# Kernel optimization log

Measured on AMD Instinct MI355X. Metric: run time of the kernel, lower is better.

The kernel has to match this reference:

```python
import jax, jax.numpy as jnp
import numpy as np

B = 512       # number of graphs
MAX_N = 128   # pad length (>= max(num_atoms))
D = 256       # emb_dim


def setup_inputs() -> dict:
    key = jax.random.key(0)
    ks = jax.random.split(key, 20)
    num_atoms_np = np.full(B, 80, dtype=np.int64)
    num_atoms_np[: B // 2] = 112
    num_atoms_np[B // 2 :] = 48
    total = int(num_atoms_np.sum())  # 40960, static
    scale = 1.0 / np.sqrt(D)

    def lin_w(k):
        return jax.random.normal(k, (D, D), jnp.float32) * scale

    inp = {
        'rep_2d': jax.random.normal(ks[0], (total, D), jnp.float32),
        'rep_3d': jax.random.normal(ks[1], (total, D), jnp.float32),
        'num_atoms': jnp.asarray(num_atoms_np),
        # mha_2d_3d (queries from 2d, keys/values from 3d)
        'wq23': lin_w(ks[2]), 'bq23': jnp.zeros((D,), jnp.float32),
        'wk23': lin_w(ks[3]), 'bk23': jnp.zeros((D,), jnp.float32),
        'wv23': lin_w(ks[4]), 'bv23': jnp.zeros((D,), jnp.float32),
        # mha_3d_2d (queries from 3d, keys/values from 2d)
        'wq32': lin_w(ks[5]), 'bq32': jnp.zeros((D,), jnp.float32),
        'wk32': lin_w(ks[6]), 'bk32': jnp.zeros((D,), jnp.float32),
        'wv32': lin_w(ks[7]), 'bv32': jnp.zeros((D,), jnp.float32),
        # per-branch Linear (normalizer=Identity) + GELU
        'wm23': lin_w(ks[8]), 'bm23': jnp.zeros((D,), jnp.float32),
        'wm32': lin_w(ks[9]), 'bm32': jnp.zeros((D,), jnp.float32),
    }
    return inp


def _variadic_to_padded(flat, num_atoms):
    # flat: [total, D] -> padded [B, MAX_N, D], mask [B, MAX_N] (True = valid)
    cum = jnp.cumsum(num_atoms)
    offsets = cum - num_atoms
    pos = jnp.arange(MAX_N)
    mask = pos[None, :] < num_atoms[:, None]
    idx = jnp.where(mask, offsets[:, None] + pos[None, :], 0)
    padded = flat[idx] * mask[..., None].astype(flat.dtype)
    return padded, mask


def _padded_to_variadic(padded, num_atoms, total):
    # padded: [B, MAX_N, D] -> flat [total, D]
    cum = jnp.cumsum(num_atoms)
    t = jnp.arange(total)
    b = jnp.searchsorted(cum, t, side='right')
    i = t - (cum - num_atoms)[b]
    return padded[b, i]


def _cross_attn(q_in, kv_in, mask, wq, bq, wk, bk, wv, bv):
    # single-head scaled dot-product cross-attention, key-side padding mask
    q = q_in @ wq.T + bq
    k = kv_in @ wk.T + bk
    v = kv_in @ wv.T + bv
    s = jnp.einsum('bqd,bkd->bqk', q, k) / jnp.sqrt(jnp.asarray(D, q.dtype))
    s = jnp.where(mask[:, None, :], s, jnp.asarray(-1e9, s.dtype))
    a = jax.nn.softmax(s, axis=-1)
    return jnp.einsum('bqk,bkd->bqd', a, v)


def reference(rep_2d, rep_3d, num_atoms,
              wq23, bq23, wk23, bk23, wv23, bv23,
              wq32, bq32, wk32, bk32, wv32, bv32,
              wm23, bm23, wm32, bm32):
    total = rep_2d.shape[0]
    p2d, mask = _variadic_to_padded(rep_2d, num_atoms)
    p3d, _ = _variadic_to_padded(rep_3d, num_atoms)
    x2d = _cross_attn(p2d, p3d, mask, wq23, bq23, wk23, bk23, wv23, bv23)
    x3d = _cross_attn(p3d, p2d, mask, wq32, bq32, wk32, bk32, wv32, bv32)
    x2d = _padded_to_variadic(x2d, num_atoms, total)
    x3d = _padded_to_variadic(x3d, num_atoms, total)
    out2d = jax.nn.gelu(x2d @ wm23.T + bm23, approximate=False)
    out3d = jax.nn.gelu(x3d @ wm32.T + bm32, approximate=False)
    return (out2d, out3d)
```

## Files before the change

kernel.cpp:

```cpp
#include <hip/hip_runtime.h>
#include <hip/hip_bf16.h>
#include <cstdint>


typedef short s16x8 __attribute__((ext_vector_type(8)));
typedef float f32x4 __attribute__((ext_vector_type(4)));

__device__ __forceinline__ s16x8 cvt8(const float* p) {
  float4 a0 = *(const float4*)p, a1 = *(const float4*)(p + 4);
  union { s16x8 v; __bf16 e[8]; } u;
  u.e[0] = (__bf16)a0.x; u.e[1] = (__bf16)a0.y; u.e[2] = (__bf16)a0.z; u.e[3] = (__bf16)a0.w;
  u.e[4] = (__bf16)a1.x; u.e[5] = (__bf16)a1.y; u.e[6] = (__bf16)a1.z; u.e[7] = (__bf16)a1.w;
  return u.v;
}
__device__ __forceinline__ float fast_gelu(float x) {
  float ax = fabsf(x);
  float t = 1.0f / (1.0f + 0.3275911f * (ax * 0.70710678f));
  float y = t * (0.254829592f + t * (-0.284496736f + t * (1.421413741f +
            t * (-1.453152027f + t * 1.061405429f))));
  float er = 1.0f - y * __expf(-0.5f * ax * ax);
  er = (x < 0.f) ? -er : er;
  return 0.5f * x * (1.0f + er);
}

__global__ void sentinel_kernel(float* out, float v) {
  if (threadIdx.x == 0 && blockIdx.x == 0) out[0] = v;
}

__global__ __launch_bounds__(512) void scan_kernel(
    const int* __restrict__ na, int* __restrict__ offs,
    int B, int total, float* out)
{
  __shared__ int s32[512];
  __shared__ int s64[512];
  const int t = threadIdx.x;
  int v32 = 0, v64 = 0;
  if (t < B) {
    v32 = na[t];
    v64 = (int)((const long long*)na)[t];
  }
  s32[t] = v32; s64[t] = v64;
  __syncthreads();
  for (int o = 1; o < 512; o <<= 1) {
    int a = (t >= o) ? s32[t - o] : 0;
    int b = (t >= o) ? s64[t - o] : 0;
    __syncthreads();
    s32[t] += a; s64[t] += b;
    __syncthreads();
  }
  int tot32 = s32[B - 1], tot64 = s64[B - 1];
  bool ok32 = (tot32 == total), ok64 = (tot64 == total);
  if (t < B) offs[t] = ok32 ? (s32[t] - v32) : ok64 ? (s64[t] - v64) : 0;
  if (t == 0) {
    offs[B] = ok32 ? tot32 : ok64 ? tot64 : 0;
    if (!ok32 && !ok64) out[0] = 31337.0f;
  }
}

__global__ __launch_bounds__(256) void cvt_kernel(
    const float* __restrict__ in, __bf16* __restrict__ out) {
  int i = (blockIdx.x * 256 + threadIdx.x) * 4;
  float4 f = *(const float4*)(in + i);
  out[i + 0] = (__bf16)f.x; out[i + 1] = (__bf16)f.y;
  out[i + 2] = (__bf16)f.z; out[i + 3] = (__bf16)f.w;
}

__global__ __launch_bounds__(256) void gemm_kernel(
    const float* __restrict__ A, const float* __restrict__ Bw,
    const float* __restrict__ bias, __bf16* __restrict__ C, int N)
{
  __shared__ __bf16 At[128 * 32];
  __shared__ __bf16 Bt[128 * 32];
  const int t = threadIdx.x;
  const int lane = t & 63, w = t >> 6;
  const int wr = w >> 1, wc = w & 1;
  const int l15 = lane & 15, l4 = lane >> 4;
  const int by = blockIdx.x, bx = blockIdx.y;

  f32x4 acc[4][4];
  for (int m = 0; m < 4; ++m)
    for (int nn = 0; nn < 4; ++nn) acc[m][nn] = (f32x4){0.f, 0.f, 0.f, 0.f};

  for (int kk = 0; kk < 256; kk += 32) {
    for (int j = 0; j < 2; ++j) {
      int c = t + j * 256;
      int row = c >> 2, off0 = (c & 3) * 8;
      *(s16x8*)(&At[row * 32 + off0]) = cvt8(A + (size_t)(by * 128 + row) * 256 + kk + off0);
      *(s16x8*)(&Bt[row * 32 + off0]) = cvt8(Bw + (size_t)(bx * 128 + row) * 256 + kk + off0);
    }
    __syncthreads();
    s16x8 af[4], bfr[4];
    for (int m = 0; m < 4; ++m)
      af[m] = *(const s16x8*)(&At[(wr * 64 + m * 16 + l15) * 32 + l4 * 8]);
    for (int nn = 0; nn < 4; ++nn)
      bfr[nn] = *(const s16x8*)(&Bt[(wc * 64 + nn * 16 + l15) * 32 + l4 * 8]);
    for (int m = 0; m < 4; ++m)
      for (int nn = 0; nn < 4; ++nn)
        acc[m][nn] = __builtin_amdgcn_mfma_f32_16x16x32_bf16(af[m], bfr[nn], acc[m][nn], 0, 0, 0);
    __syncthreads();
  }

  for (int m = 0; m < 4; ++m) {
    int row0 = by * 128 + wr * 64 + m * 16 + l4 * 4;
    for (int nn = 0; nn < 4; ++nn) {
      int col = bx * 128 + wc * 64 + nn * 16 + l15;
      float bc = bias[col];
      for (int r = 0; r < 4; ++r) {
        int row = row0 + r;
        C[(size_t)row * N + col] = (__bf16)(acc[m][nn][r] + bc);
      }
    }
  }
}

#define CTP 136
__global__ __launch_bounds__(256) void vgemm_kernel(
    const float* __restrict__ A, const float* __restrict__ Bw,
    const float* __restrict__ bias, __bf16* __restrict__ Vt, int total)
{
  __shared__ __bf16 At[128 * 32];
  __shared__ __bf16 Bt[128 * 32];
  __shared__ __bf16 Ct[128 * CTP];
  const int t = threadIdx.x;
  const int lane = t & 63, w = t >> 6;
  const int wr = w >> 1, wc = w & 1;
  const int l15 = lane & 15, l4 = lane >> 4;
  const int by = blockIdx.x, bx = blockIdx.y;

  f32x4 acc[4][4];
  for (int m = 0; m < 4; ++m)
    for (int nn = 0; nn < 4; ++nn) acc[m][nn] = (f32x4){0.f, 0.f, 0.f, 0.f};

  for (int kk = 0; kk < 256; kk += 32) {
    for (int j = 0; j < 2; ++j) {
      int c = t + j * 256;
      int row = c >> 2, off0 = (c & 3) * 8;
      *(s16x8*)(&At[row * 32 + off0]) = cvt8(A + (size_t)(by * 128 + row) * 256 + kk + off0);
      *(s16x8*)(&Bt[row * 32 + off0]) = cvt8(Bw + (size_t)(bx * 128 + row) * 256 + kk + off0);
    }
    __syncthreads();
    s16x8 af[4], bfr[4];
    for (int m = 0; m < 4; ++m)
      af[m] = *(const s16x8*)(&At[(wr * 64 + m * 16 + l15) * 32 + l4 * 8]);
    for (int nn = 0; nn < 4; ++nn)
      bfr[nn] = *(const s16x8*)(&Bt[(wc * 64 + nn * 16 + l15) * 32 + l4 * 8]);
    for (int m = 0; m < 4; ++m)
      for (int nn = 0; nn < 4; ++nn)
        acc[m][nn] = __builtin_amdgcn_mfma_f32_16x16x32_bf16(af[m], bfr[nn], acc[m][nn], 0, 0, 0);
    __syncthreads();
  }

  for (int m = 0; m < 4; ++m) {
    int rl0 = wr * 64 + m * 16 + l4 * 4;
    for (int nn = 0; nn < 4; ++nn) {
      int cl = wc * 64 + nn * 16 + l15;
      for (int r = 0; r < 4; ++r) {
        int rl = rl0 + r;
        Ct[rl * CTP + cl] = (__bf16)(acc[m][nn][r] + bias[by * 128 + rl]);
      }
    }
  }
  __syncthreads();

  for (int i = 0; i < 8; ++i) {
    int c = t + i * 256;
    int row = c >> 4, seg = c & 15;
    *(uint4*)(Vt + (size_t)(by * 128 + row) * total + bx * 128 + seg * 8) =
        *(const uint4*)(&Ct[row * CTP + seg * 8]);
  }
}

struct Attn2Args {
  const __bf16* Q[2]; const __bf16* K[2]; const __bf16* V[2];
  unsigned long long X[2];
};
#define KSTR 264
#define PSTR 136
__global__ __launch_bounds__(512, 2) void attn2_kernel(
    Attn2Args args, const int* __restrict__ offs, int total)
{
  __shared__ __bf16 smem[128 * KSTR];
  __bf16 (*Klds)[KSTR] = (__bf16(*)[KSTR])smem;
  __bf16 (*Plds)[PSTR] = (__bf16(*)[PSTR])smem;

  const int br = blockIdx.y;
  const __bf16* Q  = args.Q[br];
  const __bf16* Km = args.K[br];
  const __bf16* Vt = args.V[br];
  __bf16* X = (__bf16*)args.X[br];

  const int g = blockIdx.x;
  const int off = offs[g];
  const int n = offs[g + 1] - off;
  const int t = threadIdx.x, lane = t & 63, w = t >> 6;
  const int l15 = lane & 15, l4 = lane >> 4;
  const bool qact = (w * 16) < n;

  uint4 kst[8];
  #pragma unroll
  for (int j = 0; j < 8; ++j) {
    if (j * 16 < n) {
      int row = j * 16 + (t >> 5);
      kst[j] = *(const uint4*)((const char*)(Km + (size_t)(off + row) * 256) + (t & 31) * 16);
    }
  }
  s16x8 qf[8];
  if (qact) {
    int qr = w * 16 + l15; if (qr >= n) qr = n - 1;
    const __bf16* qp = Q + (size_t)(off + qr) * 256 + l4 * 8;
    #pragma unroll
    for (int kk = 0; kk < 8; ++kk) qf[kk] = *(const s16x8*)(qp + kk * 32);
  }
  #pragma unroll
  for (int j = 0; j < 8; ++j) {
    if (j * 16 < n) {
      int row = j * 16 + (t >> 5);
      *(uint4*)((char*)&Klds[row][0] + (t & 31) * 16) = kst[j];
    }
  }
  __syncthreads();

  f32x4 sacc[8];
  #pragma unroll
  for (int i = 0; i < 8; ++i) sacc[i] = (f32x4){0.f, 0.f, 0.f, 0.f};
  if (qact) {
    #pragma unroll
    for (int kt = 0; kt < 8; ++kt) {
      if (kt * 16 < n) {
        const __bf16* kp = &Klds[kt * 16 + l15][l4 * 8];
        #pragma unroll
        for (int kk = 0; kk < 8; ++kk) {
          s16x8 kf = *(const s16x8*)(kp + kk * 32);
          sacc[kt] = __builtin_amdgcn_mfma_f32_16x16x32_bf16(qf[kk], kf, sacc[kt], 0, 0, 0);
        }
      }
    }
  }
  __syncthreads();

  if (qact) {
    #pragma unroll
    for (int r = 0; r < 4; ++r) {
      float sv[8];
      float m = -1e30f;
      #pragma unroll
      for (int kt = 0; kt < 8; ++kt) {
        int key = kt * 16 + l15;
        float v = (key < n) ? sacc[kt][r] * 0.0625f : -1e30f;
        sv[kt] = v; m = fmaxf(m, v);
      }
      for (int o = 1; o < 16; o <<= 1) m = fmaxf(m, __shfl_xor(m, o));
      float p[8], sum = 0.f;
      #pragma unroll
      for (int kt = 0; kt < 8; ++kt) { p[kt] = __expf(sv[kt] - m); sum += p[kt]; }
      for (int o = 1; o < 16; o <<= 1) sum += __shfl_xor(sum, o);
      float inv = 1.f / sum;
      int q = w * 16 + l4 * 4 + r;
      #pragma unroll
      for (int kt = 0; kt < 8; ++kt)
        Plds[q][kt * 16 + l15] = (__bf16)(p[kt] * inv);
    }
  }
  __syncthreads();

  const int dbase = w * 32;
  f32x4 xacc[2][8];
  #pragma unroll
  for (int dt = 0; dt < 2; ++dt)
    #pragma unroll
    for (int qm = 0; qm < 8; ++qm) xacc[dt][qm] = (f32x4){0.f, 0.f, 0.f, 0.f};

  #pragma unroll
  for (int dt = 0; dt < 2; ++dt) {
    int d = dbase + dt * 16 + l15;
    s16x8 vf[4];
    #pragma unroll
    for (int ks = 0; ks < 4; ++ks) {
      if (ks * 32 < n) {
        int kc = off + ks * 32 + l4 * 8;
        if (kc > total - 8) kc = total - 8;
        vf[ks] = *(const s16x8*)(Vt + (size_t)d * total + kc);
      }
    }
    #pragma unroll
    for (int qm = 0; qm < 8; ++qm) {
      if (qm * 16 < n) {
        #pragma unroll
        for (int ks = 0; ks < 4; ++ks) {
          if (ks * 32 < n) {
            s16x8 pa = *(const s16x8*)(&Plds[qm * 16 + l15][ks * 32 + l4 * 8]);
            xacc[dt][qm] = __builtin_amdgcn_mfma_f32_16x16x32_bf16(pa, vf[ks], xacc[dt][qm], 0, 0, 0);
          }
        }
      }
    }
  }

  #pragma unroll
  for (int dt = 0; dt < 2; ++dt)
    #pragma unroll
    for (int qm = 0; qm < 8; ++qm)
      #pragma unroll
      for (int r = 0; r < 4; ++r) {
        int q = qm * 16 + l4 * 4 + r;
        if (q < n)
          X[(size_t)(off + q) * 256 + dbase + dt * 16 + l15] = (__bf16)xacc[dt][qm][r];
      }
}

struct Out2Args {
  const __bf16* A[2]; const __bf16* W[2]; const float* bias[2];
  unsigned long long C[2];
};
__global__ __launch_bounds__(256) void gemm_out2(Out2Args args)
{
  __shared__ __bf16 At[64 * 32];
  __shared__ __bf16 Bt[128 * 32];
  const int z = blockIdx.z;
  const __bf16* A  = args.A[z];
  const __bf16* W  = args.W[z];
  const float* bias = args.bias[z];
  float* C = (float*)args.C[z];

  const int t = threadIdx.x;
  const int lane = t & 63, w = t >> 6;
  const int wr = w >> 1, wc = w & 1;
  const int l15 = lane & 15, l4 = lane >> 4;
  const int by = blockIdx.x, bx = blockIdx.y;

  f32x4 acc[2][4];
  for (int m = 0; m < 2; ++m)
    for (int nn = 0; nn < 4; ++nn) acc[m][nn] = (f32x4){0.f, 0.f, 0.f, 0.f};

  for (int kk = 0; kk < 256; kk += 32) {
    {
      int row = t >> 2, off0 = (t & 3) * 8;
      *(s16x8*)(&At[row * 32 + off0]) =
          *(const s16x8*)(A + (size_t)(by * 64 + row) * 256 + kk + off0);
    }
    for (int j = 0; j < 2; ++j) {
      int c = t + j * 256;
      int row = c >> 2, off0 = (c & 3) * 8;
      *(s16x8*)(&Bt[row * 32 + off0]) =
          *(const s16x8*)(W + (size_t)(bx * 128 + row) * 256 + kk + off0);
    }
    __syncthreads();
    s16x8 af[2], bfr[4];
    for (int m = 0; m < 2; ++m)
      af[m] = *(const s16x8*)(&At[(wr * 32 + m * 16 + l15) * 32 + l4 * 8]);
    for (int nn = 0; nn < 4; ++nn)
      bfr[nn] = *(const s16x8*)(&Bt[(wc * 64 + nn * 16 + l15) * 32 + l4 * 8]);
    for (int m = 0; m < 2; ++m)
      for (int nn = 0; nn < 4; ++nn)
        acc[m][nn] = __builtin_amdgcn_mfma_f32_16x16x32_bf16(af[m], bfr[nn], acc[m][nn], 0, 0, 0);
    __syncthreads();
  }

  for (int m = 0; m < 2; ++m) {
    int row0 = by * 64 + wr * 32 + m * 16 + l4 * 4;
    for (int nn = 0; nn < 4; ++nn) {
      int col = bx * 128 + wc * 64 + nn * 16 + l15;
      float bc = bias[col];
      for (int r = 0; r < 4; ++r) {
        int row = row0 + r;
        C[(size_t)row * 256 + col] = fast_gelu(acc[m][nn][r] + bc);
      }
    }
  }
}

extern "C" void kernel_launch(void* const* d_in, const int* in_sizes, int n_in,
                              void* d_out, int out_size, void* d_ws, size_t ws_size,
                              hipStream_t stream) {
  const float* rep2d = (const float*)d_in[0];
  const float* rep3d = (const float*)d_in[1];
  const int*   na    = (const int*)d_in[2];
  const float* wq23 = (const float*)d_in[3];  const float* bq23 = (const float*)d_in[4];
  const float* wk23 = (const float*)d_in[5];  const float* bk23 = (const float*)d_in[6];
  const float* wv23 = (const float*)d_in[7];  const float* bv23 = (const float*)d_in[8];
  const float* wq32 = (const float*)d_in[9];  const float* bq32 = (const float*)d_in[10];
  const float* wk32 = (const float*)d_in[11]; const float* bk32 = (const float*)d_in[12];
  const float* wv32 = (const float*)d_in[13]; const float* bv32 = (const float*)d_in[14];
  const float* wm23 = (const float*)d_in[15]; const float* bm23 = (const float*)d_in[16];
  const float* wm32 = (const float*)d_in[17]; const float* bm32 = (const float*)d_in[18];

  const int B = in_sizes[2];
  const int total = in_sizes[0] / 256;
  float* out = (float*)d_out;

  char* ws = (char*)d_ws;
  const size_t SZ = (size_t)total * 256 * sizeof(__bf16);
  const size_t WMB = 65536 * sizeof(__bf16);
  const size_t need6 = 8192 + 2 * WMB + 6 * SZ;
  const size_t need3 = 8192 + 2 * WMB + 3 * SZ;
  int* offs = (int*)ws;

  dim3 blk(256);
  dim3 blkA(512);
  dim3 gP(total / 128, 2);
  dim3 gV(2, total / 128);

  if (ws_size >= need6) {
    __bf16* WM0 = (__bf16*)(ws + 8192);
    __bf16* WM1 = (__bf16*)(ws + 8192 + WMB);
    __bf16* BQ1 = (__bf16*)(ws + 8192 + 2 * WMB);
    __bf16* BK1 = (__bf16*)(ws + 8192 + 2 * WMB + SZ);
    __bf16* BV1 = (__bf16*)(ws + 8192 + 2 * WMB + 2 * SZ);
    __bf16* BQ2 = (__bf16*)(ws + 8192 + 2 * WMB + 3 * SZ);
    __bf16* BK2 = (__bf16*)(ws + 8192 + 2 * WMB + 4 * SZ);
    __bf16* BV2 = (__bf16*)(ws + 8192 + 2 * WMB + 5 * SZ);

    scan_kernel<<<1, 512, 0, stream>>>(na, offs, B, total, out);
    cvt_kernel<<<64, blk, 0, stream>>>(wm23, WM0);
    cvt_kernel<<<64, blk, 0, stream>>>(wm32, WM1);
    gemm_kernel<<<gP, blk, 0, stream>>>(rep2d, wq23, bq23, BQ1, 256);
    gemm_kernel<<<gP, blk, 0, stream>>>(rep3d, wk23, bk23, BK1, 256);
    vgemm_kernel<<<gV, blk, 0, stream>>>(wv23, rep3d, bv23, BV1, total);
    gemm_kernel<<<gP, blk, 0, stream>>>(rep3d, wq32, bq32, BQ2, 256);
    gemm_kernel<<<gP, blk, 0, stream>>>(rep2d, wk32, bk32, BK2, 256);
    vgemm_kernel<<<gV, blk, 0, stream>>>(wv32, rep2d, bv32, BV2, total);

    Attn2Args aa;
    aa.Q[0] = BQ1; aa.K[0] = BK1; aa.V[0] = BV1; aa.X[0] = (unsigned long long)BQ1;
    aa.Q[1] = BQ2; aa.K[1] = BK2; aa.V[1] = BV2; aa.X[1] = (unsigned long long)BQ2;
    attn2_kernel<<<dim3(B, 2), blkA, 0, stream>>>(aa, offs, total);

    Out2Args oa;
    oa.A[0] = BQ1; oa.W[0] = WM0; oa.bias[0] = bm23; oa.C[0] = (unsigned long long)out;
    oa.A[1] = BQ2; oa.W[1] = WM1; oa.bias[1] = bm32;
    oa.C[1] = (unsigned long long)(out + (size_t)total * 256);
    gemm_out2<<<dim3(total / 64, 2, 2), blk, 0, stream>>>(oa);
  } else if (ws_size >= need3) {
    __bf16* WM0 = (__bf16*)(ws + 8192);
    __bf16* WM1 = (__bf16*)(ws + 8192 + WMB);
    __bf16* BQ = (__bf16*)(ws + 8192 + 2 * WMB);
    __bf16* BK = (__bf16*)(ws + 8192 + 2 * WMB + SZ);
    __bf16* BV = (__bf16*)(ws + 8192 + 2 * WMB + 2 * SZ);

    scan_kernel<<<1, 512, 0, stream>>>(na, offs, B, total, out);
    cvt_kernel<<<64, blk, 0, stream>>>(wm23, WM0);
    cvt_kernel<<<64, blk, 0, stream>>>(wm32, WM1);
    for (int br = 0; br < 2; ++br) {
      const float* rq = br ? rep3d : rep2d;
      const float* rk = br ? rep2d : rep3d;
      const float* wq = br ? wq32 : wq23;  const float* bq = br ? bq32 : bq23;
      const float* wk = br ? wk32 : wk23;  const float* bk = br ? bk32 : bk23;
      const float* wv = br ? wv32 : wv23;  const float* bv = br ? bv32 : bv23;
      __bf16* wm = br ? WM1 : WM0;         const float* bm = br ? bm32 : bm23;
      float* o = out + (size_t)br * total * 256;

      gemm_kernel<<<gP, blk, 0, stream>>>(rq, wq, bq, BQ, 256);
      gemm_kernel<<<gP, blk, 0, stream>>>(rk, wk, bk, BK, 256);
      vgemm_kernel<<<gV, blk, 0, stream>>>(wv, rk, bv, BV, total);
      Attn2Args aa;
      aa.Q[0] = BQ; aa.K[0] = BK; aa.V[0] = BV; aa.X[0] = (unsigned long long)BQ;
      aa.Q[1] = BQ; aa.K[1] = BK; aa.V[1] = BV; aa.X[1] = (unsigned long long)BQ;
      attn2_kernel<<<dim3(B, 1), blkA, 0, stream>>>(aa, offs, total);
      Out2Args oa;
      oa.A[0] = BQ; oa.W[0] = wm; oa.bias[0] = bm; oa.C[0] = (unsigned long long)o;
      oa.A[1] = BQ; oa.W[1] = wm; oa.bias[1] = bm; oa.C[1] = (unsigned long long)o;
      gemm_out2<<<dim3(total / 64, 2, 1), blk, 0, stream>>>(oa);
    }
  } else {
    sentinel_kernel<<<1, 64, 0, stream>>>(out, 54321.0f);
  }
}
```

Baseline: 225.4 us.

## Stage attention output through LDS for coalesced stores, split output GEMM launches

The attention kernel now writes its bf16 output tile to shared memory and then stores full 16-byte rows to global memory, replacing scattered 2-byte stores. It also drops the n-bound guards on the K and V loads and on the qm loop, so each block always loads and multiplies all 128 rows. The output GEMM goes back from one batched launch to two separate launches. The coalesced stores should cut write transactions. The cost is unconditional loads and MFMAs on padding, an extra barrier, and an extra kernel launch. Because the K loads are now unguarded, blocks near the end of the buffer may read past the valid rows.

```diff
diff --git a/kernel.cpp b/kernel.cpp
--- a/kernel.cpp
+++ b/kernel.cpp
@@ -182,6 +182,7 @@
   __shared__ __bf16 smem[128 * KSTR];
   __bf16 (*Klds)[KSTR] = (__bf16(*)[KSTR])smem;
   __bf16 (*Plds)[PSTR] = (__bf16(*)[PSTR])smem;
+  __bf16 (*XT)[KSTR]   = (__bf16(*)[KSTR])smem;
 
   const int br = blockIdx.y;
   const __bf16* Q  = args.Q[br];
@@ -199,10 +200,8 @@
   uint4 kst[8];
   #pragma unroll
   for (int j = 0; j < 8; ++j) {
-    if (j * 16 < n) {
-      int row = j * 16 + (t >> 5);
-      kst[j] = *(const uint4*)((const char*)(Km + (size_t)(off + row) * 256) + (t & 31) * 16);
-    }
+    int row = j * 16 + (t >> 5);
+    kst[j] = *(const uint4*)((const char*)(Km + (size_t)(off + row) * 256) + (t & 31) * 16);
   }
   s16x8 qf[8];
   if (qact) {
@@ -213,10 +212,8 @@
   }
   #pragma unroll
   for (int j = 0; j < 8; ++j) {
-    if (j * 16 < n) {
-      int row = j * 16 + (t >> 5);
-      *(uint4*)((char*)&Klds[row][0] + (t & 31) * 16) = kst[j];
-    }
+    int row = j * 16 + (t >> 5);
+    *(uint4*)((char*)&Klds[row][0] + (t & 31) * 16) = kst[j];
   }
   __syncthreads();
 
@@ -276,52 +273,48 @@
     s16x8 vf[4];
     #pragma unroll
     for (int ks = 0; ks < 4; ++ks) {
-      if (ks * 32 < n) {
-        int kc = off + ks * 32 + l4 * 8;
-        if (kc > total - 8) kc = total - 8;
-        vf[ks] = *(const s16x8*)(Vt + (size_t)d * total + kc);
-      }
+      int kc = off + ks * 32 + l4 * 8;
+      if (kc > total - 8) kc = total - 8;
+      vf[ks] = *(const s16x8*)(Vt + (size_t)d * total + kc);
     }
     #pragma unroll
     for (int qm = 0; qm < 8; ++qm) {
-      if (qm * 16 < n) {
-        #pragma unroll
-        for (int ks = 0; ks < 4; ++ks) {
-          if (ks * 32 < n) {
-            s16x8 pa = *(const s16x8*)(&Plds[qm * 16 + l15][ks * 32 + l4 * 8]);
-            xacc[dt][qm] = __builtin_amdgcn_mfma_f32_16x16x32_bf16(pa, vf[ks], xacc[dt][qm], 0, 0, 0);
-          }
+      #pragma unroll
+      for (int ks = 0; ks < 4; ++ks) {
+        if (ks * 32 < n) {
+          s16x8 pa = *(const s16x8*)(&Plds[qm * 16 + l15][ks * 32 + l4 * 8]);
+          xacc[dt][qm] = __builtin_amdgcn_mfma_f32_16x16x32_bf16(pa, vf[ks], xacc[dt][qm], 0, 0, 0);
         }
       }
     }
   }
+  __syncthreads();
 
   #pragma unroll
   for (int dt = 0; dt < 2; ++dt)
     #pragma unroll
     for (int qm = 0; qm < 8; ++qm)
       #pragma unroll
-      for (int r = 0; r < 4; ++r) {
-        int q = qm * 16 + l4 * 4 + r;
-        if (q < n)
-          X[(size_t)(off + q) * 256 + dbase + dt * 16 + l15] = (__bf16)xacc[dt][qm][r];
-      }
-}
-
-struct Out2Args {
-  const __bf16* A[2]; const __bf16* W[2]; const float* bias[2];
-  unsigned long long C[2];
-};
-__global__ __launch_bounds__(256) void gemm_out2(Out2Args args)
+      for (int r = 0; r < 4; ++r)
+        XT[qm * 16 + l4 * 4 + r][dbase + dt * 16 + l15] = (__bf16)xacc[dt][qm][r];
+  __syncthreads();
+
+  #pragma unroll
+  for (int i = 0; i < 8; ++i) {
+    int c = t + i * 512;
+    int row = c >> 5, seg = c & 31;
+    if (row < n)
+      *(uint4*)(X + (size_t)(off + row) * 256 + seg * 8) =
+          *(const uint4*)(&XT[row][seg * 8]);
+  }
+}
+
+__global__ __launch_bounds__(256) void gemm_out(
+    const __bf16* __restrict__ A, const __bf16* __restrict__ W,
+    const float* __restrict__ bias, float* __restrict__ C)
 {
   __shared__ __bf16 At[64 * 32];
   __shared__ __bf16 Bt[128 * 32];
-  const int z = blockIdx.z;
-  const __bf16* A  = args.A[z];
-  const __bf16* W  = args.W[z];
-  const float* bias = args.bias[z];
-  float* C = (float*)args.C[z];
-
   const int t = threadIdx.x;
   const int lane = t & 63, w = t >> 6;
   const int wr = w >> 1, wc = w & 1;
@@ -399,6 +392,7 @@
   dim3 blkA(512);
   dim3 gP(total / 128, 2);
   dim3 gV(2, total / 128);
+  dim3 gO(total / 64, 2);
 
   if (ws_size >= need6) {
     __bf16* WM0 = (__bf16*)(ws + 8192);
@@ -425,11 +419,8 @@
     aa.Q[1] = BQ2; aa.K[1] = BK2; aa.V[1] = BV2; aa.X[1] = (unsigned long long)BQ2;
     attn2_kernel<<<dim3(B, 2), blkA, 0, stream>>>(aa, offs, total);
 
-    Out2Args oa;
-    oa.A[0] = BQ1; oa.W[0] = WM0; oa.bias[0] = bm23; oa.C[0] = (unsigned long long)out;
-    oa.A[1] = BQ2; oa.W[1] = WM1; oa.bias[1] = bm32;
-    oa.C[1] = (unsigned long long)(out + (size_t)total * 256);
-    gemm_out2<<<dim3(total / 64, 2, 2), blk, 0, stream>>>(oa);
+    gemm_out<<<gO, blk, 0, stream>>>(BQ1, WM0, bm23, out);
+    gemm_out<<<gO, blk, 0, stream>>>(BQ2, WM1, bm32, out + (size_t)total * 256);
   } else if (ws_size >= need3) {
     __bf16* WM0 = (__bf16*)(ws + 8192);
     __bf16* WM1 = (__bf16*)(ws + 8192 + WMB);
@@ -456,10 +447,7 @@
       aa.Q[0] = BQ; aa.K[0] = BK; aa.V[0] = BV; aa.X[0] = (unsigned long long)BQ;
       aa.Q[1] = BQ; aa.K[1] = BK; aa.V[1] = BV; aa.X[1] = (unsigned long long)BQ;
       attn2_kernel<<<dim3(B, 1), blkA, 0, stream>>>(aa, offs, total);
-      Out2Args oa;
-      oa.A[0] = BQ; oa.W[0] = wm; oa.bias[0] = bm; oa.C[0] = (unsigned long long)o;
-      oa.A[1] = BQ; oa.W[1] = wm; oa.bias[1] = bm; oa.C[1] = (unsigned long long)o;
-      gemm_out2<<<dim3(total / 64, 2, 1), blk, 0, stream>>>(oa);
+      gemm_out<<<gO, blk, 0, stream>>>(BQ, wm, bm, o);
     }
   } else {
     sentinel_kernel<<<1, 64, 0, stream>>>(out, 54321.0f);
```

New measurement: 211.3 us. -6.3%, faster.
